# Optimization experiments

Hardware: AMD Instinct MI355X
Metric: run time of the kernel (lower is better)

Reference implementation:

```python
import jax, jax.numpy as jnp
import numpy as np

B, T, I, H, L = 32768, 30, 4, 64, 32


def _lstm_layer(x, Wih, Whh, bih, bhh):
    """PyTorch-semantics single-layer LSTM, batch_first. Returns (outputs [B,T,H], h_T [B,H])."""
    # Precompute input contribution for all timesteps: [B, T, 4H]
    xg = jnp.einsum('bti,gi->btg', x, Wih) + bih + bhh
    Hh = Whh.shape[1]
    h0 = jnp.zeros((x.shape[0], Hh), x.dtype)

    def step(carry, xg_t):
        h, c = carry
        g = xg_t + h @ Whh.T  # [B, 4H]
        i, f, gg, o = jnp.split(g, 4, axis=-1)  # PyTorch gate order i,f,g,o
        c = jax.nn.sigmoid(f) * c + jax.nn.sigmoid(i) * jnp.tanh(gg)
        h = jax.nn.sigmoid(o) * jnp.tanh(c)
        return (h, c), h

    (hT, _), hs = jax.lax.scan(step, (h0, h0), jnp.swapaxes(xg, 0, 1))
    return jnp.swapaxes(hs, 0, 1), hT


def setup_inputs() -> dict:
    key = jax.random.key(0)
    ks = jax.random.split(key, 20)
    s = 0.1  # weight scale for numerical stability
    inp = {
        'x': jax.random.normal(ks[0], (B, T, I), jnp.float32),
        'enc1_Wih': s * jax.random.normal(ks[1], (4 * H, I), jnp.float32),
        'enc1_Whh': s * jax.random.normal(ks[2], (4 * H, H), jnp.float32),
        'enc1_bih': s * jax.random.normal(ks[3], (4 * H,), jnp.float32),
        'enc1_bhh': s * jax.random.normal(ks[4], (4 * H,), jnp.float32),
        'enc2_Wih': s * jax.random.normal(ks[5], (4 * L, H), jnp.float32),
        'enc2_Whh': s * jax.random.normal(ks[6], (4 * L, L), jnp.float32),
        'enc2_bih': s * jax.random.normal(ks[7], (4 * L,), jnp.float32),
        'enc2_bhh': s * jax.random.normal(ks[8], (4 * L,), jnp.float32),
        'dec1_Wih': s * jax.random.normal(ks[9], (4 * H, L), jnp.float32),
        'dec1_Whh': s * jax.random.normal(ks[10], (4 * H, H), jnp.float32),
        'dec1_bih': s * jax.random.normal(ks[11], (4 * H,), jnp.float32),
        'dec1_bhh': s * jax.random.normal(ks[12], (4 * H,), jnp.float32),
        'dec2_Wih': s * jax.random.normal(ks[13], (4 * I, H), jnp.float32),
        'dec2_Whh': s * jax.random.normal(ks[14], (4 * I, I), jnp.float32),
        'dec2_bih': s * jax.random.normal(ks[15], (4 * I,), jnp.float32),
        'dec2_bhh': s * jax.random.normal(ks[16], (4 * I,), jnp.float32),
    }
    return inp


def reference(x, enc1_Wih, enc1_Whh, enc1_bih, enc1_bhh,
              enc2_Wih, enc2_Whh, enc2_bih, enc2_bhh,
              dec1_Wih, dec1_Whh, dec1_bih, dec1_bhh,
              dec2_Wih, dec2_Whh, dec2_bih, dec2_bhh):
    seq_len = x.shape[1]
    out, _ = _lstm_layer(x, enc1_Wih, enc1_Whh, enc1_bih, enc1_bhh)
    out, h = _lstm_layer(out, enc2_Wih, enc2_Whh, enc2_bih, enc2_bhh)
    latent = jnp.repeat(h[:, None, :], seq_len, axis=1)  # [B, T, L]
    out, _ = _lstm_layer(latent, dec1_Wih, dec1_Whh, dec1_bih, dec1_bhh)
    out, _ = _lstm_layer(out, dec2_Wih, dec2_Whh, dec2_bih, dec2_bhh)
    return out
```

## Files before the change

### kernel.cpp

```cpp
#include <hip/hip_runtime.h>
#include <stdint.h>


typedef unsigned short u16;
typedef unsigned int u32;
typedef __attribute__((ext_vector_type(8))) short bf16x8;
typedef __attribute__((ext_vector_type(4))) float f32x4;
typedef __attribute__((ext_vector_type(4))) u32 u32x4;
typedef __attribute__((ext_vector_type(2))) u32 u32x2;

#define BATCH 32768
#define TT 30
#define IN 4
#define WAVES 16
#define BLOCKT (WAVES * 64)
#define MB 16
#define NPAIR 8
#define BPB (NPAIR * MB)

#define LOG2E 1.4426950408889634f
#define LOG2E2 2.8853900817779268f

#define WREG 18432
#define O_WHH1HI 0
#define O_W1FOLD 8192
#define O_WIH2HI 12288
#define O_WHH2HI 16384
#define O_WHH3HI 0
#define O_WIH3HI 8192
#define O_WIH4HI 12288
#define O_W4HHF  12800

#define NBIAS 400
#define PBUF 1600
#define SMEM_WORDS (WREG + NBIAS + NPAIR * PBUF)
#define SMEM_BYTES (SMEM_WORDS * 4)

#define WB() __builtin_amdgcn_wave_barrier()
#define MFMA(a, b, c) __builtin_amdgcn_mfma_f32_16x16x32_bf16((a), (b), (c), 0, 0, 0)

__device__ __forceinline__ u16 f2bf(float f) {
    u32 u = __float_as_uint(f);
    u += 0x7fffu + ((u >> 16) & 1u);
    return (u16)(u >> 16);
}
__device__ __forceinline__ float bf2f(u16 v) { return __uint_as_float(((u32)v) << 16); }

__device__ __forceinline__ u32 cvtpk2(float a, float b) {
    u32 d;
    asm("v_cvt_pk_bf16_f32 %0, %1, %2" : "=v"(d) : "v"(a), "v"(b));
    return d;
}

__device__ __forceinline__ float unitH(float yi, float yf, float yg, float yo, float& c) {
    const float ei = __builtin_amdgcn_exp2f(-yi);
    const float ef = __builtin_amdgcn_exp2f(-yf);
    const float eg = __builtin_amdgcn_exp2f(yg);
    const float eo = __builtin_amdgcn_exp2f(-yo);
    const float Z = (1.f + ei) * (1.f + eg);
    const float X = 1.f + ef;
    const float num = fmaf(eg - 1.f, X, c * Z);
    c = num * __builtin_amdgcn_rcpf(X * Z);
    const float ec = __builtin_amdgcn_exp2f(c * LOG2E2);
    return (ec - 1.f) * __builtin_amdgcn_rcpf((1.f + eo) * (1.f + ec));
}

template <int KT, int GS>
__device__ __forceinline__ void stageBh(u16* hi, const float* src, int N, int tid) {
    const int K = KT * 32;
    const int total = N * K;
    for (int idx = tid; idx < total; idx += BLOCKT) {
        const int j = idx & 7;
        const int l = (idx >> 3) & 63;
        const int pr = idx >> 9;
        const int kt = pr & (KT - 1);
        const int nt = pr / KT;
        const int n = (nt << 4) | (l & 15);
        const int k = (kt << 5) + ((l >> 4) << 3) + j;
        const float s = (((n >> GS) & 3) == 2) ? LOG2E2 : LOG2E;
        hi[idx] = f2bf(src[n * K + k] * s);
    }
}

__global__ __launch_bounds__(BLOCKT)
__attribute__((amdgpu_waves_per_eu(4, 4)))
void lstm_ae(
    const float* __restrict__ x,
    const float* __restrict__ w1ih, const float* __restrict__ w1hh,
    const float* __restrict__ b1i, const float* __restrict__ b1h,
    const float* __restrict__ w2ih, const float* __restrict__ w2hh,
    const float* __restrict__ b2i, const float* __restrict__ b2h,
    const float* __restrict__ w3ih, const float* __restrict__ w3hh,
    const float* __restrict__ b3i, const float* __restrict__ b3h,
    const float* __restrict__ w4ih, const float* __restrict__ w4hh,
    const float* __restrict__ b4i, const float* __restrict__ b4h,
    float* __restrict__ out) {
    extern __shared__ float smem[];
    float* W = smem;
    float* biasF = smem + WREG;
    float* bufs = biasF + NBIAS;

    const int tid = threadIdx.x;
    const int wave = tid >> 6, lane = tid & 63;
    const int pair = wave & 7, role = wave >> 3;
    const int col = lane & 15, quad = lane >> 4;

    float* pb = bufs + pair * PBUF;
    u16* h1d = (u16*)pb;
    u16* h2b = (u16*)(pb + 1024);
    float* gbuf = pb + 1280;
    float* bufH4 = pb + 1536;

    const int b0w = blockIdx.x * BPB + pair * MB;
    const int hbase = (col << 3) + ((quad & 1) << 2) + ((quad >> 1) << 7);

    stageBh<2, 6>((u16*)(W + O_WHH1HI), w1hh, 256, tid);
    stageBh<2, 5>((u16*)(W + O_WIH2HI), w2ih, 128, tid);
    stageBh<1, 5>((u16*)(W + O_WHH2HI), w2hh, 128, tid);
    {
        u16* F = (u16*)(W + O_W1FOLD);
        for (int idx = tid; idx < 16 * 512; idx += BLOCKT) {
            const int nt = idx >> 9;
            const int rem = idx & 511;
            const int l = rem >> 3;
            const int j = rem & 7;
            const int q = l >> 4;
            const int n = (nt << 4) | (l & 15);
            const float s = ((n >> 6) == 2) ? LOG2E2 : LOG2E;
            u16 v = 0;
            if (q == 0) {
                v = f2bf(w1ih[n * 4 + (j & 3)] * s);
            } else if (q == 1) {
                if (j < 4) {
                    const float w = w1ih[n * 4 + j] * s;
                    v = f2bf(w - bf2f(f2bf(w)));
                } else if (j == 4) {
                    v = f2bf((b1i[n] + b1h[n]) * s);
                } else if (j == 5) {
                    const float b = (b1i[n] + b1h[n]) * s;
                    v = f2bf(b - bf2f(f2bf(b)));
                }
            }
            F[idx] = v;
        }
    }
    for (int i = tid; i < 128; i += BLOCKT)
        biasF[i] = (b2i[i] + b2h[i]) * ((((i >> 5) & 3) == 2) ? LOG2E2 : LOG2E);
    for (int i = tid; i < 256; i += BLOCKT)
        biasF[128 + i] = (b3i[i] + b3h[i]) * ((((i >> 6) & 3) == 2) ? LOG2E2 : LOG2E);
    for (int i = tid; i < 16; i += BLOCKT)
        biasF[384 + i] = (b4i[i] + b4h[i]) * ((((i >> 2) & 3) == 2) ? LOG2E2 : LOG2E);
    {
        u32* z = (u32*)pb;
        if (role == 0) {
            for (int i = lane; i < 1024; i += 64) z[i] = 0u;
        } else {
            for (int i = lane; i < 256; i += 64) z[1024 + i] = 0u;
            bufH4[lane] = 0.f;
        }
    }
    __syncthreads();

    const u16* Whh1hi = (const u16*)(W + O_WHH1HI);
    const u16* W1fold = (const u16*)(W + O_W1FOLD);
    const u16* Wih2hi = (const u16*)(W + O_WIH2HI);
    const u16* Whh2hi = (const u16*)(W + O_WHH2HI);

    float c1[4][4];
    float c2[2][4];
#pragma unroll
    for (int q = 0; q < 4; ++q)
#pragma unroll
        for (int r = 0; r < 4; ++r) c1[q][r] = 0.f;
#pragma unroll
    for (int q = 0; q < 2; ++q)
#pragma unroll
        for (int r = 0; r < 4; ++r) c2[q][r] = 0.f;

    const f32x4 zf = {0.f, 0.f, 0.f, 0.f};
    float4 xcur;
    if (role == 0)
        xcur = *reinterpret_cast<const float4*>(x + ((size_t)(b0w + col) * TT + 0) * IN);

    for (int s = 0; s <= TT; ++s) {
        if (role == 0) {
            if (s < TT) {
                const u32 hi01 = cvtpk2(xcur.x, xcur.y);
                const u32 hi23 = cvtpk2(xcur.z, xcur.w);
                const float r0 = xcur.x - __uint_as_float(hi01 << 16);
                const float r1 = xcur.y - __uint_as_float(hi01 & 0xffff0000u);
                const float r2 = xcur.z - __uint_as_float(hi23 << 16);
                const float r3 = xcur.w - __uint_as_float(hi23 & 0xffff0000u);
                const u32 lo01 = cvtpk2(r0, r1);
                const u32 lo23 = cvtpk2(r2, r3);
                u32x4 xv;
                xv.x = (quad <= 1) ? hi01 : 0u;
                xv.y = (quad <= 1) ? hi23 : 0u;
                xv.z = (quad == 0) ? lo01 : ((quad == 1) ? 0x3F803F80u : 0u);
                xv.w = (quad == 0) ? lo23 : 0u;
                const bf16x8 a1x = __builtin_bit_cast(bf16x8, xv);
                {
                    const int tn = (s + 1 < TT) ? s + 1 : s;
                    xcur = *reinterpret_cast<const float4*>(
                        x + ((size_t)(b0w + col) * TT + tn) * IN);
                }
                const u16* hprev = h1d + (((s + 1) & 1) << 10);
                u16* hout = h1d + ((s & 1) << 10);
                const bf16x8 a1h0 = *reinterpret_cast<const bf16x8*>(hprev + lane * 8);
                const bf16x8 a1h1 = *reinterpret_cast<const bf16x8*>(hprev + (64 + lane) * 8);
#pragma unroll
                for (int q = 0; q < 4; ++q) {
                    f32x4 acc[4];
#pragma unroll
                    for (int i = 0; i < 4; ++i) {
                        const int nt = i * 4 + q;
                        const bf16x8 bx = *reinterpret_cast<const bf16x8*>(W1fold + (nt * 64 + lane) * 8);
                        const bf16x8 bh0 = *reinterpret_cast<const bf16x8*>(Whh1hi + ((nt * 2 + 0) * 64 + lane) * 8);
                        const bf16x8 bh1 = *reinterpret_cast<const bf16x8*>(Whh1hi + ((nt * 2 + 1) * 64 + lane) * 8);
                        f32x4 a = MFMA(bx, a1x, zf);
                        a = MFMA(bh0, a1h0, a);
                        a = MFMA(bh1, a1h1, a);
                        acc[i] = a;
                    }
                    const float h0 = unitH(acc[0][0], acc[1][0], acc[2][0], acc[3][0], c1[q][0]);
                    const float h1 = unitH(acc[0][1], acc[1][1], acc[2][1], acc[3][1], c1[q][1]);
                    const float h2 = unitH(acc[0][2], acc[1][2], acc[2][2], acc[3][2], c1[q][2]);
                    const float h3 = unitH(acc[0][3], acc[1][3], acc[2][3], acc[3][3], c1[q][3]);
                    u32x2 wv;
                    wv.x = cvtpk2(h0, h1);
                    wv.y = cvtpk2(h2, h3);
                    *reinterpret_cast<u32x2*>(hout + hbase + ((q >> 1) << 9) + ((q & 1) << 8)) = wv;
                }
            }
        } else {
            if (s >= 1) {
                const u16* hprev = h1d + (((s + 1) & 1) << 10);
                const bf16x8 a1h0 = *reinterpret_cast<const bf16x8*>(hprev + lane * 8);
                const bf16x8 a1h1 = *reinterpret_cast<const bf16x8*>(hprev + (64 + lane) * 8);
                const bf16x8 a2h = *reinterpret_cast<const bf16x8*>(h2b + lane * 8);
                f32x4 acc2[8];
#pragma unroll
                for (int nt = 0; nt < 8; ++nt) {
                    const bf16x8 bh0 = *reinterpret_cast<const bf16x8*>(Wih2hi + ((nt * 2 + 0) * 64 + lane) * 8);
                    const bf16x8 bh1 = *reinterpret_cast<const bf16x8*>(Wih2hi + ((nt * 2 + 1) * 64 + lane) * 8);
                    const bf16x8 ch = *reinterpret_cast<const bf16x8*>(Whh2hi + (nt * 64 + lane) * 8);
                    f32x4 a = *reinterpret_cast<const f32x4*>(biasF + nt * 16 + (quad << 2));
                    a = MFMA(bh0, a1h0, a);
                    a = MFMA(bh1, a1h1, a);
                    a = MFMA(ch, a2h, a);
                    acc2[nt] = a;
                }
                WB();
#pragma unroll
                for (int q = 0; q < 2; ++q) {
                    const float h0 = unitH(acc2[q][0], acc2[2 + q][0], acc2[4 + q][0], acc2[6 + q][0], c2[q][0]);
                    const float h1 = unitH(acc2[q][1], acc2[2 + q][1], acc2[4 + q][1], acc2[6 + q][1], c2[q][1]);
                    const float h2 = unitH(acc2[q][2], acc2[2 + q][2], acc2[4 + q][2], acc2[6 + q][2], c2[q][2]);
                    const float h3 = unitH(acc2[q][3], acc2[2 + q][3], acc2[4 + q][3], acc2[6 + q][3], c2[q][3]);
                    u32x2 wv;
                    wv.x = cvtpk2(h0, h1);
                    wv.y = cvtpk2(h2, h3);
                    *reinterpret_cast<u32x2*>(h2b + hbase + (q << 8)) = wv;
                }
            }
        }
        __syncthreads();
    }

    stageBh<2, 6>((u16*)(W + O_WHH3HI), w3hh, 256, tid);
    stageBh<1, 6>((u16*)(W + O_WIH3HI), w3ih, 256, tid);
    stageBh<2, 2>((u16*)(W + O_WIH4HI), w4ih, 16, tid);
    for (int i = tid; i < 64; i += BLOCKT)
        W[O_W4HHF + i] = w4hh[i] * ((((i >> 4) & 3) == 2) ? LOG2E2 : LOG2E);
    if (role == 0) {
        u32* z = (u32*)pb;
        for (int i = lane; i < 1024; i += 64) z[i] = 0u;
    } else {
        bufH4[lane] = 0.f;
    }
    __syncthreads();

    const u16* Whh3hi = (const u16*)(W + O_WHH3HI);
    const u16* Wih3hi = (const u16*)(W + O_WIH3HI);
    const u16* Wih4hi = (const u16*)(W + O_WIH4HI);
    const float* W4hhF = W + O_W4HHF;

    float c3[4][4];
    float c4 = 0.f;
    f32x4 bias4v = zf;
    bf16x8 aLh;
    if (role == 0) {
#pragma unroll
        for (int q = 0; q < 4; ++q)
#pragma unroll
            for (int r = 0; r < 4; ++r) c3[q][r] = 0.f;
        aLh = *reinterpret_cast<const bf16x8*>(h2b + lane * 8);
    } else {
        bias4v = *reinterpret_cast<const f32x4*>(biasF + 384 + (quad << 2));
    }
    const int u4 = lane & 3, mb = lane >> 2;

    for (int s = 0; s <= TT; ++s) {
        if (role == 0) {
            if (s < TT) {
                const u16* hprev = h1d + (((s + 1) & 1) << 10);
                u16* hout = h1d + ((s & 1) << 10);
                const bf16x8 a3h0 = *reinterpret_cast<const bf16x8*>(hprev + lane * 8);
                const bf16x8 a3h1 = *reinterpret_cast<const bf16x8*>(hprev + (64 + lane) * 8);
#pragma unroll
                for (int q = 0; q < 4; ++q) {
                    f32x4 acc[4];
#pragma unroll
                    for (int i = 0; i < 4; ++i) {
                        const int nt = i * 4 + q;
                        const bf16x8 bL = *reinterpret_cast<const bf16x8*>(Wih3hi + (nt * 64 + lane) * 8);
                        const bf16x8 bh0 = *reinterpret_cast<const bf16x8*>(Whh3hi + ((nt * 2 + 0) * 64 + lane) * 8);
                        const bf16x8 bh1 = *reinterpret_cast<const bf16x8*>(Whh3hi + ((nt * 2 + 1) * 64 + lane) * 8);
                        f32x4 a = *reinterpret_cast<const f32x4*>(biasF + 128 + nt * 16 + (quad << 2));
                        a = MFMA(bL, aLh, a);
                        a = MFMA(bh0, a3h0, a);
                        a = MFMA(bh1, a3h1, a);
                        acc[i] = a;
                    }
                    const float h0 = unitH(acc[0][0], acc[1][0], acc[2][0], acc[3][0], c3[q][0]);
                    const float h1 = unitH(acc[0][1], acc[1][1], acc[2][1], acc[3][1], c3[q][1]);
                    const float h2 = unitH(acc[0][2], acc[1][2], acc[2][2], acc[3][2], c3[q][2]);
                    const float h3 = unitH(acc[0][3], acc[1][3], acc[2][3], acc[3][3], c3[q][3]);
                    u32x2 wv;
                    wv.x = cvtpk2(h0, h1);
                    wv.y = cvtpk2(h2, h3);
                    *reinterpret_cast<u32x2*>(hout + hbase + ((q >> 1) << 9) + ((q & 1) << 8)) = wv;
                }
            }
        } else {
            if (s >= 1) {
                const int t = s - 1;
                const u16* hprev = h1d + (((s + 1) & 1) << 10);
                const bf16x8 a3h0 = *reinterpret_cast<const bf16x8*>(hprev + lane * 8);
                const bf16x8 a3h1 = *reinterpret_cast<const bf16x8*>(hprev + (64 + lane) * 8);
                f32x4 acc4 = bias4v;
                {
                    const float4 hv = *reinterpret_cast<const float4*>(bufH4 + (col << 2));
#pragma unroll
                    for (int r = 0; r < 4; ++r) {
                        const float4 w4 = *reinterpret_cast<const float4*>(W4hhF + ((quad * 4 + r) << 2));
                        float sa = acc4[r];
                        sa = fmaf(w4.x, hv.x, sa);
                        sa = fmaf(w4.y, hv.y, sa);
                        sa = fmaf(w4.z, hv.z, sa);
                        sa = fmaf(w4.w, hv.w, sa);
                        acc4[r] = sa;
                    }
                }
                {
                    const bf16x8 bh0 = *reinterpret_cast<const bf16x8*>(Wih4hi + (0 * 64 + lane) * 8);
                    const bf16x8 bh1 = *reinterpret_cast<const bf16x8*>(Wih4hi + (1 * 64 + lane) * 8);
                    acc4 = MFMA(bh0, a3h0, acc4);
                    acc4 = MFMA(bh1, a3h1, acc4);
                }
                WB();
                *reinterpret_cast<f32x4*>(gbuf + (col << 4) + (quad << 2)) = acc4;
                WB();
                {
                    const float yi = gbuf[mb * 16 + u4];
                    const float yf = gbuf[mb * 16 + 4 + u4];
                    const float yg = gbuf[mb * 16 + 8 + u4];
                    const float yo = gbuf[mb * 16 + 12 + u4];
                    const float h = unitH(yi, yf, yg, yo, c4);
                    out[((size_t)(b0w + mb) * TT + t) * IN + u4] = h;
                    bufH4[mb * 4 + u4] = h;
                }
                WB();
            }
        }
        __syncthreads();
    }
}

extern "C" void kernel_launch(void* const* d_in, const int* in_sizes, int n_in,
                              void* d_out, int out_size, void* d_ws, size_t ws_size,
                              hipStream_t stream) {
    (void)in_sizes; (void)n_in; (void)d_ws; (void)ws_size; (void)out_size;
    hipFuncSetAttribute(reinterpret_cast<const void*>(lstm_ae),
                        hipFuncAttributeMaxDynamicSharedMemorySize, SMEM_BYTES);
    const float* xi = (const float*)d_in[0];
    const float* w1ih = (const float*)d_in[1];
    const float* w1hh = (const float*)d_in[2];
    const float* b1i = (const float*)d_in[3];
    const float* b1h = (const float*)d_in[4];
    const float* w2ih = (const float*)d_in[5];
    const float* w2hh = (const float*)d_in[6];
    const float* b2i = (const float*)d_in[7];
    const float* b2h = (const float*)d_in[8];
    const float* w3ih = (const float*)d_in[9];
    const float* w3hh = (const float*)d_in[10];
    const float* b3i = (const float*)d_in[11];
    const float* b3h = (const float*)d_in[12];
    const float* w4ih = (const float*)d_in[13];
    const float* w4hh = (const float*)d_in[14];
    const float* b4i = (const float*)d_in[15];
    const float* b4h = (const float*)d_in[16];
    float* out = (float*)d_out;

    lstm_ae<<<dim3(BATCH / BPB), dim3(BLOCKT), SMEM_BYTES, stream>>>(
        xi, w1ih, w1hh, b1i, b1h, w2ih, w2hh, b2i, b2h,
        w3ih, w3hh, b3i, b3h, w4ih, w4hh, b4i, b4h, out);
}
```

Before: 289.1 us.

## Run each wave through both layers serially, dropping pair-split and block barriers

Replaces the producer/consumer wave-pair split, where one wave ran layer 1 and a partner wave ran layer 2 one step behind with a block-wide __syncthreads each step, with one wave per 16-sample batch tile that computes both stacked layers in sequence. Only wave-local barriers remain inside the time loop. The block shrinks to 8 waves, per-wave LDS buffers shrink because h1 no longer needs double buffering, and the layer-1 input/bias fold is replaced by a compact weight table plus an fp32 bias accumulator init. This removes per-step block barriers and cross-wave skew, at the cost of the two layers' MFMA chains no longer running in parallel within a batch tile. Occupancy hints also change (waves_per_eu 2).

```diff
diff --git a/kernel.cpp b/kernel.cpp
--- a/kernel.cpp
+++ b/kernel.cpp
@@ -12,28 +12,29 @@
 #define BATCH 32768
 #define TT 30
 #define IN 4
-#define WAVES 16
+#define WAVES 8
 #define BLOCKT (WAVES * 64)
 #define MB 16
-#define NPAIR 8
-#define BPB (NPAIR * MB)
+#define BPB (WAVES * MB)
 
 #define LOG2E 1.4426950408889634f
 #define LOG2E2 2.8853900817779268f
 
-#define WREG 18432
-#define O_WHH1HI 0
-#define O_W1FOLD 8192
-#define O_WIH2HI 12288
-#define O_WHH2HI 16384
-#define O_WHH3HI 0
-#define O_WIH3HI 8192
-#define O_WIH4HI 12288
-#define O_W4HHF  12800
-
-#define NBIAS 400
-#define PBUF 1600
-#define SMEM_WORDS (WREG + NBIAS + NPAIR * PBUF)
+#define O_WHH1 0
+#define O_W1C  8192
+#define O_WIH2 9216
+#define O_WHH2 13312
+#define O_WHH3 0
+#define O_WIH3 8192
+#define O_WIH4 12288
+#define O_W4HHF 12800
+#define O_B1F 15360
+#define O_B2F 15616
+#define O_B3F 15744
+#define O_B4F 16000
+#define O_BUFS 16016
+#define PBUF 1088
+#define SMEM_WORDS (O_BUFS + WAVES * PBUF)
 #define SMEM_BYTES (SMEM_WORDS * 4)
 
 #define WB() __builtin_amdgcn_wave_barrier()
@@ -83,7 +84,7 @@
 }
 
 __global__ __launch_bounds__(BLOCKT)
-__attribute__((amdgpu_waves_per_eu(4, 4)))
+__attribute__((amdgpu_waves_per_eu(2)))
 void lstm_ae(
     const float* __restrict__ x,
     const float* __restrict__ w1ih, const float* __restrict__ w1hh,
@@ -97,74 +98,54 @@
     float* __restrict__ out) {
     extern __shared__ float smem[];
     float* W = smem;
-    float* biasF = smem + WREG;
-    float* bufs = biasF + NBIAS;
 
     const int tid = threadIdx.x;
     const int wave = tid >> 6, lane = tid & 63;
-    const int pair = wave & 7, role = wave >> 3;
     const int col = lane & 15, quad = lane >> 4;
 
-    float* pb = bufs + pair * PBUF;
-    u16* h1d = (u16*)pb;
-    u16* h2b = (u16*)(pb + 1024);
-    float* gbuf = pb + 1280;
-    float* bufH4 = pb + 1536;
-
-    const int b0w = blockIdx.x * BPB + pair * MB;
+    float* pb = smem + O_BUFS + wave * PBUF;
+    u16* h1b = (u16*)pb;
+    u16* h2b = (u16*)(pb + 512);
+    float* gbuf = pb + 768;
+    float* bufH4 = pb + 1024;
+
+    const int b0w = blockIdx.x * BPB + wave * MB;
     const int hbase = (col << 3) + ((quad & 1) << 2) + ((quad >> 1) << 7);
 
-    stageBh<2, 6>((u16*)(W + O_WHH1HI), w1hh, 256, tid);
-    stageBh<2, 5>((u16*)(W + O_WIH2HI), w2ih, 128, tid);
-    stageBh<1, 5>((u16*)(W + O_WHH2HI), w2hh, 128, tid);
+    stageBh<2, 6>((u16*)(W + O_WHH1), w1hh, 256, tid);
+    stageBh<2, 5>((u16*)(W + O_WIH2), w2ih, 128, tid);
+    stageBh<1, 5>((u16*)(W + O_WHH2), w2hh, 128, tid);
     {
-        u16* F = (u16*)(W + O_W1FOLD);
-        for (int idx = tid; idx < 16 * 512; idx += BLOCKT) {
-            const int nt = idx >> 9;
-            const int rem = idx & 511;
-            const int l = rem >> 3;
-            const int j = rem & 7;
-            const int q = l >> 4;
-            const int n = (nt << 4) | (l & 15);
-            const float s = ((n >> 6) == 2) ? LOG2E2 : LOG2E;
-            u16 v = 0;
-            if (q == 0) {
-                v = f2bf(w1ih[n * 4 + (j & 3)] * s);
-            } else if (q == 1) {
-                if (j < 4) {
-                    const float w = w1ih[n * 4 + j] * s;
-                    v = f2bf(w - bf2f(f2bf(w)));
-                } else if (j == 4) {
-                    v = f2bf((b1i[n] + b1h[n]) * s);
-                } else if (j == 5) {
-                    const float b = (b1i[n] + b1h[n]) * s;
-                    v = f2bf(b - bf2f(f2bf(b)));
-                }
-            }
-            F[idx] = v;
-        }
-    }
+        u16* C = (u16*)(W + O_W1C);
+        for (int idx = tid; idx < 2048; idx += BLOCKT) {
+            const int n = idx >> 3, j = idx & 7;
+            const float sc = ((n >> 6) == 2) ? LOG2E2 : LOG2E;
+            const float w = w1ih[n * 4 + (j & 3)] * sc;
+            C[idx] = (j < 4) ? f2bf(w) : f2bf(w - bf2f(f2bf(w)));
+        }
+    }
+    float* b1f = W + O_B1F;
+    float* b2f = W + O_B2F;
+    float* b3f = W + O_B3F;
+    float* b4f = W + O_B4F;
+    for (int i = tid; i < 256; i += BLOCKT)
+        b1f[i] = (b1i[i] + b1h[i]) * (((i >> 6) == 2) ? LOG2E2 : LOG2E);
     for (int i = tid; i < 128; i += BLOCKT)
-        biasF[i] = (b2i[i] + b2h[i]) * ((((i >> 5) & 3) == 2) ? LOG2E2 : LOG2E);
+        b2f[i] = (b2i[i] + b2h[i]) * (((i >> 5) == 2) ? LOG2E2 : LOG2E);
     for (int i = tid; i < 256; i += BLOCKT)
-        biasF[128 + i] = (b3i[i] + b3h[i]) * ((((i >> 6) & 3) == 2) ? LOG2E2 : LOG2E);
+        b3f[i] = (b3i[i] + b3h[i]) * (((i >> 6) == 2) ? LOG2E2 : LOG2E);
     for (int i = tid; i < 16; i += BLOCKT)
-        biasF[384 + i] = (b4i[i] + b4h[i]) * ((((i >> 2) & 3) == 2) ? LOG2E2 : LOG2E);
+        b4f[i] = (b4i[i] + b4h[i]) * (((i >> 2) == 2) ? LOG2E2 : LOG2E);
     {
         u32* z = (u32*)pb;
-        if (role == 0) {
-            for (int i = lane; i < 1024; i += 64) z[i] = 0u;
-        } else {
-            for (int i = lane; i < 256; i += 64) z[1024 + i] = 0u;
-            bufH4[lane] = 0.f;
-        }
+        for (int i = lane; i < 768; i += 64) z[i] = 0u;
     }
     __syncthreads();
 
-    const u16* Whh1hi = (const u16*)(W + O_WHH1HI);
-    const u16* W1fold = (const u16*)(W + O_W1FOLD);
-    const u16* Wih2hi = (const u16*)(W + O_WIH2HI);
-    const u16* Whh2hi = (const u16*)(W + O_WHH2HI);
+    const u16* Whh1hi = (const u16*)(W + O_WHH1);
+    const u16* Wih2hi = (const u16*)(W + O_WIH2);
+    const u16* Whh2hi = (const u16*)(W + O_WHH2);
+    const u16* W1cL = (const u16*)(W + O_W1C) + (col << 3) + ((quad == 1) ? 4 : 0);
 
     float c1[4][4];
     float c2[2][4];
@@ -177,203 +158,178 @@
 #pragma unroll
         for (int r = 0; r < 4; ++r) c2[q][r] = 0.f;
 
-    const f32x4 zf = {0.f, 0.f, 0.f, 0.f};
-    float4 xcur;
-    if (role == 0)
-        xcur = *reinterpret_cast<const float4*>(x + ((size_t)(b0w + col) * TT + 0) * IN);
-
-    for (int s = 0; s <= TT; ++s) {
-        if (role == 0) {
-            if (s < TT) {
-                const u32 hi01 = cvtpk2(xcur.x, xcur.y);
-                const u32 hi23 = cvtpk2(xcur.z, xcur.w);
-                const float r0 = xcur.x - __uint_as_float(hi01 << 16);
-                const float r1 = xcur.y - __uint_as_float(hi01 & 0xffff0000u);
-                const float r2 = xcur.z - __uint_as_float(hi23 << 16);
-                const float r3 = xcur.w - __uint_as_float(hi23 & 0xffff0000u);
-                const u32 lo01 = cvtpk2(r0, r1);
-                const u32 lo23 = cvtpk2(r2, r3);
-                u32x4 xv;
-                xv.x = (quad <= 1) ? hi01 : 0u;
-                xv.y = (quad <= 1) ? hi23 : 0u;
-                xv.z = (quad == 0) ? lo01 : ((quad == 1) ? 0x3F803F80u : 0u);
-                xv.w = (quad == 0) ? lo23 : 0u;
-                const bf16x8 a1x = __builtin_bit_cast(bf16x8, xv);
-                {
-                    const int tn = (s + 1 < TT) ? s + 1 : s;
-                    xcur = *reinterpret_cast<const float4*>(
-                        x + ((size_t)(b0w + col) * TT + tn) * IN);
-                }
-                const u16* hprev = h1d + (((s + 1) & 1) << 10);
-                u16* hout = h1d + ((s & 1) << 10);
-                const bf16x8 a1h0 = *reinterpret_cast<const bf16x8*>(hprev + lane * 8);
-                const bf16x8 a1h1 = *reinterpret_cast<const bf16x8*>(hprev + (64 + lane) * 8);
-#pragma unroll
-                for (int q = 0; q < 4; ++q) {
-                    f32x4 acc[4];
-#pragma unroll
-                    for (int i = 0; i < 4; ++i) {
-                        const int nt = i * 4 + q;
-                        const bf16x8 bx = *reinterpret_cast<const bf16x8*>(W1fold + (nt * 64 + lane) * 8);
-                        const bf16x8 bh0 = *reinterpret_cast<const bf16x8*>(Whh1hi + ((nt * 2 + 0) * 64 + lane) * 8);
-                        const bf16x8 bh1 = *reinterpret_cast<const bf16x8*>(Whh1hi + ((nt * 2 + 1) * 64 + lane) * 8);
-                        f32x4 a = MFMA(bx, a1x, zf);
-                        a = MFMA(bh0, a1h0, a);
-                        a = MFMA(bh1, a1h1, a);
-                        acc[i] = a;
-                    }
-                    const float h0 = unitH(acc[0][0], acc[1][0], acc[2][0], acc[3][0], c1[q][0]);
-                    const float h1 = unitH(acc[0][1], acc[1][1], acc[2][1], acc[3][1], c1[q][1]);
-                    const float h2 = unitH(acc[0][2], acc[1][2], acc[2][2], acc[3][2], c1[q][2]);
-                    const float h3 = unitH(acc[0][3], acc[1][3], acc[2][3], acc[3][3], c1[q][3]);
-                    u32x2 wv;
-                    wv.x = cvtpk2(h0, h1);
-                    wv.y = cvtpk2(h2, h3);
-                    *reinterpret_cast<u32x2*>(hout + hbase + ((q >> 1) << 9) + ((q & 1) << 8)) = wv;
-                }
+    float4 xcur = *reinterpret_cast<const float4*>(x + ((size_t)(b0w + col) * TT + 0) * IN);
+
+    for (int s = 0; s < TT; ++s) {
+        const u32 hi01 = cvtpk2(xcur.x, xcur.y);
+        const u32 hi23 = cvtpk2(xcur.z, xcur.w);
+        const float r0 = xcur.x - __uint_as_float(hi01 << 16);
+        const float r1 = xcur.y - __uint_as_float(hi01 & 0xffff0000u);
+        const float r2 = xcur.z - __uint_as_float(hi23 << 16);
+        const float r3 = xcur.w - __uint_as_float(hi23 & 0xffff0000u);
+        const u32 lo01 = cvtpk2(r0, r1);
+        const u32 lo23 = cvtpk2(r2, r3);
+        u32x4 xv;
+        xv.x = (quad <= 1) ? hi01 : 0u;
+        xv.y = (quad <= 1) ? hi23 : 0u;
+        xv.z = (quad == 0) ? lo01 : 0u;
+        xv.w = (quad == 0) ? lo23 : 0u;
+        const bf16x8 a1x = __builtin_bit_cast(bf16x8, xv);
+        {
+            const int tn = (s + 1 < TT) ? s + 1 : s;
+            xcur = *reinterpret_cast<const float4*>(x + ((size_t)(b0w + col) * TT + tn) * IN);
+        }
+        const bf16x8 a1h0 = *reinterpret_cast<const bf16x8*>(h1b + lane * 8);
+        const bf16x8 a1h1 = *reinterpret_cast<const bf16x8*>(h1b + (64 + lane) * 8);
+#pragma unroll
+        for (int q = 0; q < 4; ++q) {
+            f32x4 acc[4];
+#pragma unroll
+            for (int i = 0; i < 4; ++i) {
+                const int nt = i * 4 + q;
+                const u32x2 wp = *reinterpret_cast<const u32x2*>(W1cL + nt * 128);
+                u32x4 afu;
+                afu.x = wp.x; afu.y = wp.y; afu.z = wp.x; afu.w = wp.y;
+                const bf16x8 af = __builtin_bit_cast(bf16x8, afu);
+                const bf16x8 bh0 = *reinterpret_cast<const bf16x8*>(Whh1hi + ((nt * 2 + 0) * 64 + lane) * 8);
+                const bf16x8 bh1 = *reinterpret_cast<const bf16x8*>(Whh1hi + ((nt * 2 + 1) * 64 + lane) * 8);
+                f32x4 a = *reinterpret_cast<const f32x4*>(b1f + nt * 16 + (quad << 2));
+                a = MFMA(af, a1x, a);
+                a = MFMA(bh0, a1h0, a);
+                a = MFMA(bh1, a1h1, a);
+                acc[i] = a;
             }
-        } else {
-            if (s >= 1) {
-                const u16* hprev = h1d + (((s + 1) & 1) << 10);
-                const bf16x8 a1h0 = *reinterpret_cast<const bf16x8*>(hprev + lane * 8);
-                const bf16x8 a1h1 = *reinterpret_cast<const bf16x8*>(hprev + (64 + lane) * 8);
-                const bf16x8 a2h = *reinterpret_cast<const bf16x8*>(h2b + lane * 8);
-                f32x4 acc2[8];
-#pragma unroll
-                for (int nt = 0; nt < 8; ++nt) {
-                    const bf16x8 bh0 = *reinterpret_cast<const bf16x8*>(Wih2hi + ((nt * 2 + 0) * 64 + lane) * 8);
-                    const bf16x8 bh1 = *reinterpret_cast<const bf16x8*>(Wih2hi + ((nt * 2 + 1) * 64 + lane) * 8);
-                    const bf16x8 ch = *reinterpret_cast<const bf16x8*>(Whh2hi + (nt * 64 + lane) * 8);
-                    f32x4 a = *reinterpret_cast<const f32x4*>(biasF + nt * 16 + (quad << 2));
-                    a = MFMA(bh0, a1h0, a);
-                    a = MFMA(bh1, a1h1, a);
-                    a = MFMA(ch, a2h, a);
-                    acc2[nt] = a;
-                }
-                WB();
-#pragma unroll
-                for (int q = 0; q < 2; ++q) {
-                    const float h0 = unitH(acc2[q][0], acc2[2 + q][0], acc2[4 + q][0], acc2[6 + q][0], c2[q][0]);
-                    const float h1 = unitH(acc2[q][1], acc2[2 + q][1], acc2[4 + q][1], acc2[6 + q][1], c2[q][1]);
-                    const float h2 = unitH(acc2[q][2], acc2[2 + q][2], acc2[4 + q][2], acc2[6 + q][2], c2[q][2]);
-                    const float h3 = unitH(acc2[q][3], acc2[2 + q][3], acc2[4 + q][3], acc2[6 + q][3], c2[q][3]);
-                    u32x2 wv;
-                    wv.x = cvtpk2(h0, h1);
-                    wv.y = cvtpk2(h2, h3);
-                    *reinterpret_cast<u32x2*>(h2b + hbase + (q << 8)) = wv;
-                }
-            }
-        }
-        __syncthreads();
-    }
-
-    stageBh<2, 6>((u16*)(W + O_WHH3HI), w3hh, 256, tid);
-    stageBh<1, 6>((u16*)(W + O_WIH3HI), w3ih, 256, tid);
-    stageBh<2, 2>((u16*)(W + O_WIH4HI), w4ih, 16, tid);
+            const float h0 = unitH(acc[0][0], acc[1][0], acc[2][0], acc[3][0], c1[q][0]);
+            const float h1 = unitH(acc[0][1], acc[1][1], acc[2][1], acc[3][1], c1[q][1]);
+            const float h2 = unitH(acc[0][2], acc[1][2], acc[2][2], acc[3][2], c1[q][2]);
+            const float h3 = unitH(acc[0][3], acc[1][3], acc[2][3], acc[3][3], c1[q][3]);
+            u32x2 wv;
+            wv.x = cvtpk2(h0, h1);
+            wv.y = cvtpk2(h2, h3);
+            *reinterpret_cast<u32x2*>(h1b + hbase + ((q >> 1) << 9) + ((q & 1) << 8)) = wv;
+        }
+        WB();
+        const bf16x8 e1h0 = *reinterpret_cast<const bf16x8*>(h1b + lane * 8);
+        const bf16x8 e1h1 = *reinterpret_cast<const bf16x8*>(h1b + (64 + lane) * 8);
+        const bf16x8 a2h = *reinterpret_cast<const bf16x8*>(h2b + lane * 8);
+        f32x4 acc2[8];
+#pragma unroll
+        for (int nt = 0; nt < 8; ++nt) {
+            const bf16x8 bh0 = *reinterpret_cast<const bf16x8*>(Wih2hi + ((nt * 2 + 0) * 64 + lane) * 8);
+            const bf16x8 bh1 = *reinterpret_cast<const bf16x8*>(Wih2hi + ((nt * 2 + 1) * 64 + lane) * 8);
+            const bf16x8 ch = *reinterpret_cast<const bf16x8*>(Whh2hi + (nt * 64 + lane) * 8);
+            f32x4 a = *reinterpret_cast<const f32x4*>(b2f + nt * 16 + (quad << 2));
+            a = MFMA(bh0, e1h0, a);
+            a = MFMA(bh1, e1h1, a);
+            a = MFMA(ch, a2h, a);
+            acc2[nt] = a;
+        }
+        WB();
+#pragma unroll
+        for (int q = 0; q < 2; ++q) {
+            const float h0 = unitH(acc2[q][0], acc2[2 + q][0], acc2[4 + q][0], acc2[6 + q][0], c2[q][0]);
+            const float h1 = unitH(acc2[q][1], acc2[2 + q][1], acc2[4 + q][1], acc2[6 + q][1], c2[q][1]);
+            const float h2 = unitH(acc2[q][2], acc2[2 + q][2], acc2[4 + q][2], acc2[6 + q][2], c2[q][2]);
+            const float h3 = unitH(acc2[q][3], acc2[2 + q][3], acc2[4 + q][3], acc2[6 + q][3], c2[q][3]);
+            u32x2 wv;
+            wv.x = cvtpk2(h0, h1);
+            wv.y = cvtpk2(h2, h3);
+            *reinterpret_cast<u32x2*>(h2b + hbase + (q << 8)) = wv;
+        }
+        WB();
+    }
+
+    __syncthreads();
+    stageBh<2, 6>((u16*)(W + O_WHH3), w3hh, 256, tid);
+    stageBh<1, 6>((u16*)(W + O_WIH3), w3ih, 256, tid);
+    stageBh<2, 2>((u16*)(W + O_WIH4), w4ih, 16, tid);
     for (int i = tid; i < 64; i += BLOCKT)
         W[O_W4HHF + i] = w4hh[i] * ((((i >> 4) & 3) == 2) ? LOG2E2 : LOG2E);
-    if (role == 0) {
+
+    const bf16x8 aLh = *reinterpret_cast<const bf16x8*>(h2b + lane * 8);
+    {
         u32* z = (u32*)pb;
-        for (int i = lane; i < 1024; i += 64) z[i] = 0u;
-    } else {
+        for (int i = lane; i < 512; i += 64) z[i] = 0u;
         bufH4[lane] = 0.f;
     }
+    float c3[4][4];
+#pragma unroll
+    for (int q = 0; q < 4; ++q)
+#pragma unroll
+        for (int r = 0; r < 4; ++r) c3[q][r] = 0.f;
+    float c4 = 0.f;
+    const f32x4 bias4v = *reinterpret_cast<const f32x4*>(b4f + (quad << 2));
+    const int u4 = lane & 3, mb = lane >> 2;
     __syncthreads();
 
-    const u16* Whh3hi = (const u16*)(W + O_WHH3HI);
-    const u16* Wih3hi = (const u16*)(W + O_WIH3HI);
-    const u16* Wih4hi = (const u16*)(W + O_WIH4HI);
+    const u16* Whh3hi = (const u16*)(W + O_WHH3);
+    const u16* Wih3hi = (const u16*)(W + O_WIH3);
+    const u16* Wih4hi = (const u16*)(W + O_WIH4);
     const float* W4hhF = W + O_W4HHF;
 
-    float c3[4][4];
-    float c4 = 0.f;
-    f32x4 bias4v = zf;
-    bf16x8 aLh;
-    if (role == 0) {
-#pragma unroll
-        for (int q = 0; q < 4; ++q)
-#pragma unroll
-            for (int r = 0; r < 4; ++r) c3[q][r] = 0.f;
-        aLh = *reinterpret_cast<const bf16x8*>(h2b + lane * 8);
-    } else {
-        bias4v = *reinterpret_cast<const f32x4*>(biasF + 384 + (quad << 2));
-    }
-    const int u4 = lane & 3, mb = lane >> 2;
-
-    for (int s = 0; s <= TT; ++s) {
-        if (role == 0) {
-            if (s < TT) {
-                const u16* hprev = h1d + (((s + 1) & 1) << 10);
-                u16* hout = h1d + ((s & 1) << 10);
-                const bf16x8 a3h0 = *reinterpret_cast<const bf16x8*>(hprev + lane * 8);
-                const bf16x8 a3h1 = *reinterpret_cast<const bf16x8*>(hprev + (64 + lane) * 8);
-#pragma unroll
-                for (int q = 0; q < 4; ++q) {
-                    f32x4 acc[4];
-#pragma unroll
-                    for (int i = 0; i < 4; ++i) {
-                        const int nt = i * 4 + q;
-                        const bf16x8 bL = *reinterpret_cast<const bf16x8*>(Wih3hi + (nt * 64 + lane) * 8);
-                        const bf16x8 bh0 = *reinterpret_cast<const bf16x8*>(Whh3hi + ((nt * 2 + 0) * 64 + lane) * 8);
-                        const bf16x8 bh1 = *reinterpret_cast<const bf16x8*>(Whh3hi + ((nt * 2 + 1) * 64 + lane) * 8);
-                        f32x4 a = *reinterpret_cast<const f32x4*>(biasF + 128 + nt * 16 + (quad << 2));
-                        a = MFMA(bL, aLh, a);
-                        a = MFMA(bh0, a3h0, a);
-                        a = MFMA(bh1, a3h1, a);
-                        acc[i] = a;
-                    }
-                    const float h0 = unitH(acc[0][0], acc[1][0], acc[2][0], acc[3][0], c3[q][0]);
-                    const float h1 = unitH(acc[0][1], acc[1][1], acc[2][1], acc[3][1], c3[q][1]);
-                    const float h2 = unitH(acc[0][2], acc[1][2], acc[2][2], acc[3][2], c3[q][2]);
-                    const float h3 = unitH(acc[0][3], acc[1][3], acc[2][3], acc[3][3], c3[q][3]);
-                    u32x2 wv;
-                    wv.x = cvtpk2(h0, h1);
-                    wv.y = cvtpk2(h2, h3);
-                    *reinterpret_cast<u32x2*>(hout + hbase + ((q >> 1) << 9) + ((q & 1) << 8)) = wv;
-                }
+    for (int s = 0; s < TT; ++s) {
+        const bf16x8 a3h0 = *reinterpret_cast<const bf16x8*>(h1b + lane * 8);
+        const bf16x8 a3h1 = *reinterpret_cast<const bf16x8*>(h1b + (64 + lane) * 8);
+#pragma unroll
+        for (int q = 0; q < 4; ++q) {
+            f32x4 acc[4];
+#pragma unroll
+            for (int i = 0; i < 4; ++i) {
+                const int nt = i * 4 + q;
+                const bf16x8 bL = *reinterpret_cast<const bf16x8*>(Wih3hi + (nt * 64 + lane) * 8);
+                const bf16x8 bh0 = *reinterpret_cast<const bf16x8*>(Whh3hi + ((nt * 2 + 0) * 64 + lane) * 8);
+                const bf16x8 bh1 = *reinterpret_cast<const bf16x8*>(Whh3hi + ((nt * 2 + 1) * 64 + lane) * 8);
+                f32x4 a = *reinterpret_cast<const f32x4*>(b3f + nt * 16 + (quad << 2));
+                a = MFMA(bL, aLh, a);
+                a = MFMA(bh0, a3h0, a);
+                a = MFMA(bh1, a3h1, a);
+                acc[i] = a;
             }
-        } else {
-            if (s >= 1) {
-                const int t = s - 1;
-                const u16* hprev = h1d + (((s + 1) & 1) << 10);
-                const bf16x8 a3h0 = *reinterpret_cast<const bf16x8*>(hprev + lane * 8);
-                const bf16x8 a3h1 = *reinterpret_cast<const bf16x8*>(hprev + (64 + lane) * 8);
-                f32x4 acc4 = bias4v;
-                {
-                    const float4 hv = *reinterpret_cast<const float4*>(bufH4 + (col << 2));
-#pragma unroll
-                    for (int r = 0; r < 4; ++r) {
-                        const float4 w4 = *reinterpret_cast<const float4*>(W4hhF + ((quad * 4 + r) << 2));
-                        float sa = acc4[r];
-                        sa = fmaf(w4.x, hv.x, sa);
-                        sa = fmaf(w4.y, hv.y, sa);
-                        sa = fmaf(w4.z, hv.z, sa);
-                        sa = fmaf(w4.w, hv.w, sa);
-                        acc4[r] = sa;
-                    }
-                }
-                {
-                    const bf16x8 bh0 = *reinterpret_cast<const bf16x8*>(Wih4hi + (0 * 64 + lane) * 8);
-                    const bf16x8 bh1 = *reinterpret_cast<const bf16x8*>(Wih4hi + (1 * 64 + lane) * 8);
-                    acc4 = MFMA(bh0, a3h0, acc4);
-                    acc4 = MFMA(bh1, a3h1, acc4);
-                }
-                WB();
-                *reinterpret_cast<f32x4*>(gbuf + (col << 4) + (quad << 2)) = acc4;
-                WB();
-                {
-                    const float yi = gbuf[mb * 16 + u4];
-                    const float yf = gbuf[mb * 16 + 4 + u4];
-                    const float yg = gbuf[mb * 16 + 8 + u4];
-                    const float yo = gbuf[mb * 16 + 12 + u4];
-                    const float h = unitH(yi, yf, yg, yo, c4);
-                    out[((size_t)(b0w + mb) * TT + t) * IN + u4] = h;
-                    bufH4[mb * 4 + u4] = h;
-                }
-                WB();
+            const float h0 = unitH(acc[0][0], acc[1][0], acc[2][0], acc[3][0], c3[q][0]);
+            const float h1 = unitH(acc[0][1], acc[1][1], acc[2][1], acc[3][1], c3[q][1]);
+            const float h2 = unitH(acc[0][2], acc[1][2], acc[2][2], acc[3][2], c3[q][2]);
+            const float h3 = unitH(acc[0][3], acc[1][3], acc[2][3], acc[3][3], c3[q][3]);
+            u32x2 wv;
+            wv.x = cvtpk2(h0, h1);
+            wv.y = cvtpk2(h2, h3);
+            *reinterpret_cast<u32x2*>(h1b + hbase + ((q >> 1) << 9) + ((q & 1) << 8)) = wv;
+        }
+        WB();
+        const bf16x8 d3h0 = *reinterpret_cast<const bf16x8*>(h1b + lane * 8);
+        const bf16x8 d3h1 = *reinterpret_cast<const bf16x8*>(h1b + (64 + lane) * 8);
+        f32x4 acc4 = bias4v;
+        {
+            const float4 hv = *reinterpret_cast<const float4*>(bufH4 + (col << 2));
+#pragma unroll
+            for (int r = 0; r < 4; ++r) {
+                const float4 w4 = *reinterpret_cast<const float4*>(W4hhF + ((quad * 4 + r) << 2));
+                float sa = acc4[r];
+                sa = fmaf(w4.x, hv.x, sa);
+                sa = fmaf(w4.y, hv.y, sa);
+                sa = fmaf(w4.z, hv.z, sa);
+                sa = fmaf(w4.w, hv.w, sa);
+                acc4[r] = sa;
             }
         }
-        __syncthreads();
+        {
+            const bf16x8 bh0 = *reinterpret_cast<const bf16x8*>(Wih4hi + (0 * 64 + lane) * 8);
+            const bf16x8 bh1 = *reinterpret_cast<const bf16x8*>(Wih4hi + (1 * 64 + lane) * 8);
+            acc4 = MFMA(bh0, d3h0, acc4);
+            acc4 = MFMA(bh1, d3h1, acc4);
+        }
+        WB();
+        *reinterpret_cast<f32x4*>(gbuf + (col << 4) + (quad << 2)) = acc4;
+        WB();
+        {
+            const float yi = gbuf[mb * 16 + u4];
+            const float yf = gbuf[mb * 16 + 4 + u4];
+            const float yg = gbuf[mb * 16 + 8 + u4];
+            const float yo = gbuf[mb * 16 + 12 + u4];
+            const float h = unitH(yi, yf, yg, yo, c4);
+            out[((size_t)(b0w + mb) * TT + s) * IN + u4] = h;
+            bufH4[mb * 4 + u4] = h;
+        }
+        WB();
     }
 }
 
```

Result: slower. 311.3 us (+7.7%).
